# Performance work log

Measured on AMD Instinct MI355X. Metric: run time of the kernel, lower is better.

## Reference

```python
import jax, jax.numpy as jnp
import numpy as np

M = 8192          # flattened tokens (batch*seq)
IN_FEATURES = 4096
OUT_FEATURES = 4096


def setup_inputs() -> dict:
    key = jax.random.key(0)
    k1, k2, k3 = jax.random.split(key, 3)
    # int8-valued activations and weights, stored as int32 (values in [-128, 127])
    x = jax.random.randint(k1, (M, IN_FEATURES), -128, 128, dtype=jnp.int32)
    int_weight = jax.random.randint(k2, (OUT_FEATURES, IN_FEATURES), -128, 127, dtype=jnp.int32)
    bias = (jax.random.normal(k3, (OUT_FEATURES,), dtype=jnp.float32) * 0.02).astype(jnp.float16)
    return {"x": x, "int_weight": int_weight, "bias": bias}


def reference(x, int_weight, bias):
    # x.to(torch.int8); quik int8Matmul: int8 GEMM with int32 accumulation, out = x @ W^T
    x_i8 = x.astype(jnp.int8)
    w_i8 = int_weight.astype(jnp.int8)
    acc = jax.lax.dot_general(
        x_i8, w_i8,
        dimension_numbers=(((1,), (1,)), ((), ())),  # [M, K] x [N, K] -> [M, N]
        preferred_element_type=jnp.int32,
    )
    # .to(torch.float16) then bias add (fused epilogue target)
    return acc.astype(jnp.float16) + bias
```

## Files before the change

kernel.cpp:

```cpp
#include <hip/hip_runtime.h>

#define MDIM 8192
#define NDIM 4096
#define KDIM 4096
#define BM 256
#define BN 256
#define BK 128

typedef int v4i __attribute__((ext_vector_type(4)));
typedef int v16i __attribute__((ext_vector_type(16)));

__device__ __forceinline__ unsigned pack4(int x, int y, int z, int w) {
    return (unsigned)(x & 0xff) | ((unsigned)(y & 0xff) << 8) |
           ((unsigned)(z & 0xff) << 16) | ((unsigned)w << 24);
}

__global__ __launch_bounds__(256) void pack_tiled(const int* __restrict__ x,
                                                  const int* __restrict__ w,
                                                  uint4* __restrict__ xp,
                                                  uint4* __restrict__ wp) {
    __shared__ unsigned lds32[256 * 33];
    const int wg  = blockIdx.x;
    const int tid = threadIdx.x;
    const int kq   = tid & 31;
    const int rsub = tid >> 5;

    const int* src;
    uint4* dst;
    if (wg < 1024) {
        const int mtile = wg >> 5, kiter = wg & 31;
        src = x + (size_t)(mtile * 256) * KDIM + kiter * 128;
        dst = xp + (size_t)(mtile * 32 + kiter) * 2048;
    } else {
        const int ntile = (wg - 1024) >> 5, kiter = wg & 31;
        src = w + (size_t)(ntile * 256) * KDIM + kiter * 128;
        dst = wp + (size_t)(ntile * 32 + kiter) * 2048;
    }
#pragma unroll
    for (int it = 0; it < 32; ++it) {
        const int row = it * 8 + rsub;
        int4 v = *(const int4*)(src + (size_t)row * KDIM + kq * 4);
        lds32[row * 33 + kq] = pack4(v.x, v.y, v.z, v.w);
    }
    __syncthreads();
#pragma unroll
    for (int it = 0; it < 8; ++it) {
        const int g = it * 256 + tid;
        const int kb = g >> 8, row = g & 255;
        const unsigned* p = &lds32[row * 33 + kb * 4];
        uint4 o;
        o.x = p[0]; o.y = p[1]; o.z = p[2]; o.w = p[3];
        dst[g] = o;
    }
}

__global__ __launch_bounds__(512, 2) void gemm_i8_olp(const char* __restrict__ Ap,
                                                      const char* __restrict__ Bp,
                                                      const _Float16* __restrict__ bias,
                                                      _Float16* __restrict__ out) {
    __shared__ __align__(16) char lds[131072];

    const int tid  = threadIdx.x;
    const int lane = tid & 63;
    const int wave = tid >> 6;
    const int wr   = wave >> 2;
    const int wcn  = wave & 3;
    const int l31  = lane & 31;
    const int kg   = lane >> 5;

    const int lid = blockIdx.y * 16 + blockIdx.x;
    const int xc  = lid & 7, ii = lid >> 3;
    const int bx  = (xc & 3) * 4 + (ii & 3);
    const int by  = (xc >> 2) * 16 + (ii >> 2);
    const int bm0 = by * BM;
    const int bn0 = bx * BN;

    const char* apan = Ap + (size_t)by * (BM * KDIM) + tid * 16;
    const char* bpan = Bp + (size_t)bx * (BN * KDIM) + tid * 16;

    int aoff[4], boff[2];
#pragma unroll
    for (int mt = 0; mt < 4; ++mt)
        aoff[mt] = (wr * 128 + mt * 32 + l31) * 16 + kg * 4096;
#pragma unroll
    for (int nt = 0; nt < 2; ++nt)
        boff[nt] = (wcn * 64 + nt * 32 + l31) * 16 + kg * 4096;

    v16i acc[4][2];
#pragma unroll
    for (int mt = 0; mt < 4; ++mt)
#pragma unroll
        for (int nt = 0; nt < 2; ++nt)
#pragma unroll
            for (int i = 0; i < 16; ++i) acc[mt][nt][i] = 0;

    auto stageA = [&](int nb, const char* p) {
#pragma unroll
        for (int c2 = 0; c2 < 4; ++c2)
            __builtin_amdgcn_global_load_lds(
                (__attribute__((address_space(1))) const void*)(p + c2 * 8192),
                (__attribute__((address_space(3))) void*)(lds + nb + c2 * 8192 + tid * 16),
                16, 0, 0);
    };
    auto stageB = [&](int nb, const char* p) {
#pragma unroll
        for (int c2 = 0; c2 < 4; ++c2)
            __builtin_amdgcn_global_load_lds(
                (__attribute__((address_space(1))) const void*)(p + c2 * 8192),
                (__attribute__((address_space(3))) void*)(lds + nb + 32768 + c2 * 8192 + tid * 16),
                16, 0, 0);
    };

    auto mfma8 = [&](const v4i (&af)[4], const v4i (&bfk)[2]) {
        __builtin_amdgcn_s_setprio(1);
#pragma unroll
        for (int mt = 0; mt < 4; ++mt)
#pragma unroll
            for (int nt = 0; nt < 2; ++nt)
                acc[mt][nt] = __builtin_amdgcn_mfma_i32_32x32x32_i8(
                    af[mt], bfk[nt], acc[mt][nt], 0, 0, 0);
        __builtin_amdgcn_s_setprio(0);
    };

    auto tile = [&](int base, int nb, bool stg) {
        asm volatile("s_waitcnt vmcnt(0)" ::: "memory");
        __builtin_amdgcn_s_barrier();
        __builtin_amdgcn_sched_barrier(0);
        if (stg) {
            stageA(nb, apan);
            stageB(nb, bpan);
            apan += BM * BK;
            bpan += BN * BK;
        }
        v4i bf[2][4];
#pragma unroll
        for (int nt = 0; nt < 2; ++nt)
#pragma unroll
            for (int ks = 0; ks < 4; ++ks)
                bf[nt][ks] = *(const v4i*)(lds + base + 32768 + ks * 8192 + boff[nt]);
        v4i afA[4], afB[4];
#pragma unroll
        for (int mt = 0; mt < 4; ++mt)
            afA[mt] = *(const v4i*)(lds + base + aoff[mt]);
        __builtin_amdgcn_sched_barrier(0);
#pragma unroll
        for (int mt = 0; mt < 4; ++mt)
            afB[mt] = *(const v4i*)(lds + base + 8192 + aoff[mt]);
        __builtin_amdgcn_sched_barrier(0);
        {
            v4i bfk[2] = {bf[0][0], bf[1][0]};
            mfma8(afA, bfk);
        }
#pragma unroll
        for (int mt = 0; mt < 4; ++mt)
            afA[mt] = *(const v4i*)(lds + base + 16384 + aoff[mt]);
        __builtin_amdgcn_sched_barrier(0);
        {
            v4i bfk[2] = {bf[0][1], bf[1][1]};
            mfma8(afB, bfk);
        }
#pragma unroll
        for (int mt = 0; mt < 4; ++mt)
            afB[mt] = *(const v4i*)(lds + base + 24576 + aoff[mt]);
        __builtin_amdgcn_sched_barrier(0);
        {
            v4i bfk[2] = {bf[0][2], bf[1][2]};
            mfma8(afA, bfk);
        }
        {
            v4i bfk[2] = {bf[0][3], bf[1][3]};
            mfma8(afB, bfk);
        }
    };

    stageA(0, apan);
    stageB(0, bpan);
    apan += BM * BK;
    bpan += BN * BK;

#pragma unroll 1
    for (int t = 0; t < 31; ++t) {
        const int base = (t & 1) ? 65536 : 0;
        tile(base, base ^ 65536, true);
    }
    tile(65536, 0, false);

    const _Float16 bv0 = bias[bn0 + wcn * 64 + l31];
    const _Float16 bv1 = bias[bn0 + wcn * 64 + 32 + l31];
#pragma unroll
    for (int mt = 0; mt < 4; ++mt) {
#pragma unroll
        for (int nt = 0; nt < 2; ++nt) {
            const int gcol = bn0 + wcn * 64 + nt * 32 + l31;
            const _Float16 bb = nt ? bv1 : bv0;
#pragma unroll
            for (int r = 0; r < 16; ++r) {
                const int rit  = (r & 3) + 8 * (r >> 2) + 4 * kg;
                const int grow = bm0 + wr * 128 + mt * 32 + rit;
                _Float16 h = (_Float16)(float)acc[mt][nt][r] + bb;
                out[(size_t)grow * NDIM + gcol] = h;
            }
        }
    }
}

__global__ __launch_bounds__(256, 2) void gemm_i8_fb(const int* __restrict__ A32,
                                                     const int* __restrict__ B32,
                                                     const _Float16* __restrict__ bias,
                                                     _Float16* __restrict__ out) {
    __shared__ char lds[32768];
    const int tid  = threadIdx.x;
    const int lane = tid & 63;
    const int wave = tid >> 6;
    const int bm0 = blockIdx.y * 256;
    const int bn0 = blockIdx.x * 128;
    const int wr  = wave >> 1;
    const int wc  = wave & 1;
    const int l31 = lane & 31;
    const int kg  = lane >> 5;

    int abase[4];
#pragma unroll
    for (int mt = 0; mt < 4; ++mt)
        abase[mt] = kg * 4096 + (wr * 128 + mt * 32 + l31) * 16;

    v16i acc[4][2];
#pragma unroll
    for (int mt = 0; mt < 4; ++mt)
#pragma unroll
        for (int nt = 0; nt < 2; ++nt)
#pragma unroll
            for (int i = 0; i < 16; ++i) acc[mt][nt][i] = 0;

    int aoffs[8];
#pragma unroll
    for (int r = 0; r < 8; ++r) {
        const int c = r * 4 + wave;
        aoffs[r] = (bm0 + (c & 3) * 64 + lane) * KDIM + (c >> 2) * 16;
    }
    for (int k0 = 0; k0 < KDIM; k0 += 128) {
        v4i bfx[2][4];
#pragma unroll
        for (int r = 0; r < 8; ++r) {
            const int c = r * 4 + wave;
            const int4* s = (const int4*)(A32 + (size_t)aoffs[r]);
            int4 v0 = s[0], v1 = s[1], v2 = s[2], v3 = s[3];
            uint4 pk;
            pk.x = pack4(v0.x, v0.y, v0.z, v0.w);
            pk.y = pack4(v1.x, v1.y, v1.z, v1.w);
            pk.z = pack4(v2.x, v2.y, v2.z, v2.w);
            pk.w = pack4(v3.x, v3.y, v3.z, v3.w);
            *(uint4*)(lds + c * 1024 + lane * 16) = pk;
            aoffs[r] += 128;
        }
#pragma unroll
        for (int nt = 0; nt < 2; ++nt)
#pragma unroll
            for (int ks = 0; ks < 4; ++ks) {
                const int* s = B32 + (size_t)(bn0 + wc * 64 + nt * 32 + l31) * KDIM
                               + k0 + (2 * ks + kg) * 16;
                int4 v0 = ((const int4*)s)[0], v1 = ((const int4*)s)[1];
                int4 v2 = ((const int4*)s)[2], v3 = ((const int4*)s)[3];
                bfx[nt][ks][0] = (int)pack4(v0.x, v0.y, v0.z, v0.w);
                bfx[nt][ks][1] = (int)pack4(v1.x, v1.y, v1.z, v1.w);
                bfx[nt][ks][2] = (int)pack4(v2.x, v2.y, v2.z, v2.w);
                bfx[nt][ks][3] = (int)pack4(v3.x, v3.y, v3.z, v3.w);
            }
        __syncthreads();
#pragma unroll
        for (int ks = 0; ks < 4; ++ks) {
            v4i afr[4];
#pragma unroll
            for (int mt = 0; mt < 4; ++mt)
                afr[mt] = *(const v4i*)(lds + abase[mt] + ks * 8192);
#pragma unroll
            for (int mt = 0; mt < 4; ++mt)
#pragma unroll
                for (int nt = 0; nt < 2; ++nt)
                    acc[mt][nt] = __builtin_amdgcn_mfma_i32_32x32x32_i8(
                        afr[mt], bfx[nt][ks], acc[mt][nt], 0, 0, 0);
        }
        __syncthreads();
    }

    const _Float16 bv0 = bias[bn0 + wc * 64 + l31];
    const _Float16 bv1 = bias[bn0 + wc * 64 + 32 + l31];
#pragma unroll
    for (int mt = 0; mt < 4; ++mt) {
#pragma unroll
        for (int nt = 0; nt < 2; ++nt) {
            const int gcol = bn0 + wc * 64 + nt * 32 + l31;
            const _Float16 bb = nt ? bv1 : bv0;
#pragma unroll
            for (int r = 0; r < 16; ++r) {
                const int rit  = (r & 3) + 8 * (r >> 2) + 4 * kg;
                const int grow = bm0 + wr * 128 + mt * 32 + rit;
                _Float16 h = (_Float16)(float)acc[mt][nt][r] + bb;
                out[(size_t)grow * NDIM + gcol] = h;
            }
        }
    }
}

extern "C" void kernel_launch(void* const* d_in, const int* in_sizes, int n_in,
                              void* d_out, int out_size, void* d_ws, size_t ws_size,
                              hipStream_t stream) {
    const int* x = (const int*)d_in[0];
    const int* w = (const int*)d_in[1];
    const _Float16* bias = (const _Float16*)d_in[2];
    _Float16* out = (_Float16*)d_out;

    const size_t xbytes = (size_t)MDIM * KDIM;
    const size_t wbytes = (size_t)NDIM * KDIM;

    if (ws_size >= xbytes + wbytes) {
        char* xp = (char*)d_ws;
        char* wp = xp + xbytes;
        pack_tiled<<<1536, 256, 0, stream>>>(x, w, (uint4*)xp, (uint4*)wp);
        gemm_i8_olp<<<dim3(NDIM / BN, MDIM / BM), 512, 0, stream>>>(
            (const char*)xp, (const char*)wp, bias, out);
    } else {
        gemm_i8_fb<<<dim3(NDIM / 128, MDIM / 256), 256, 0, stream>>>(
            x, w, bias, out);
    }
}
```

Baseline: 381.5 us.

## Load B fragments directly from global into registers, halve LDS buffers

The GEMM main loop no longer stages the B (weight) tile through LDS. Each wave now loads its B fragments straight from global memory into registers, split into early and late halves, while only A is double-buffered in LDS. LDS use drops from 128 KB to 64 KB, and A reads and MFMAs are software-pipelined across tile boundaries. The aim is to cut LDS traffic and footprint. In exchange, B global loads are duplicated across the waves of a block, and their latency is now exposed inside the compute schedule.

```diff
diff --git a/kernel.cpp b/kernel.cpp
--- a/kernel.cpp
+++ b/kernel.cpp
@@ -54,11 +54,11 @@
     }
 }
 
-__global__ __launch_bounds__(512, 2) void gemm_i8_olp(const char* __restrict__ Ap,
-                                                      const char* __restrict__ Bp,
-                                                      const _Float16* __restrict__ bias,
-                                                      _Float16* __restrict__ out) {
-    __shared__ __align__(16) char lds[131072];
+__global__ __launch_bounds__(512, 2) void gemm_i8_pipe(const char* __restrict__ Ap,
+                                                       const char* __restrict__ Bp,
+                                                       const _Float16* __restrict__ bias,
+                                                       _Float16* __restrict__ out) {
+    __shared__ __align__(16) char lds[65536];
 
     const int tid  = threadIdx.x;
     const int lane = tid & 63;
@@ -76,15 +76,15 @@
     const int bn0 = bx * BN;
 
     const char* apan = Ap + (size_t)by * (BM * KDIM) + tid * 16;
-    const char* bpan = Bp + (size_t)bx * (BN * KDIM) + tid * 16;
-
-    int aoff[4], boff[2];
+    const char* bpan = Bp + (size_t)bx * (BN * KDIM);
+
+    int aoff[4], boffG[2];
 #pragma unroll
     for (int mt = 0; mt < 4; ++mt)
         aoff[mt] = (wr * 128 + mt * 32 + l31) * 16 + kg * 4096;
 #pragma unroll
     for (int nt = 0; nt < 2; ++nt)
-        boff[nt] = (wcn * 64 + nt * 32 + l31) * 16 + kg * 4096;
+        boffG[nt] = (wcn * 64 + nt * 32 + l31) * 16 + kg * 4096;
 
     v16i acc[4][2];
 #pragma unroll
@@ -94,96 +94,96 @@
 #pragma unroll
             for (int i = 0; i < 16; ++i) acc[mt][nt][i] = 0;
 
-    auto stageA = [&](int nb, const char* p) {
+    v4i afP[4], afQ[4];
+    v4i bfE[2][2], bfL[2][2];
+
+    auto stageA = [&](int nb) {
 #pragma unroll
         for (int c2 = 0; c2 < 4; ++c2)
             __builtin_amdgcn_global_load_lds(
-                (__attribute__((address_space(1))) const void*)(p + c2 * 8192),
+                (__attribute__((address_space(1))) const void*)(apan + c2 * 8192),
                 (__attribute__((address_space(3))) void*)(lds + nb + c2 * 8192 + tid * 16),
                 16, 0, 0);
     };
-    auto stageB = [&](int nb, const char* p) {
-#pragma unroll
-        for (int c2 = 0; c2 < 4; ++c2)
-            __builtin_amdgcn_global_load_lds(
-                (__attribute__((address_space(1))) const void*)(p + c2 * 8192),
-                (__attribute__((address_space(3))) void*)(lds + nb + 32768 + c2 * 8192 + tid * 16),
-                16, 0, 0);
+    auto loadB2 = [&](v4i (&d)[2][2], int ksb) {
+#pragma unroll
+        for (int nt = 0; nt < 2; ++nt)
+#pragma unroll
+            for (int k = 0; k < 2; ++k)
+                d[nt][k] = *(const v4i*)(bpan + boffG[nt] + (ksb + k) * 8192);
     };
-
-    auto mfma8 = [&](const v4i (&af)[4], const v4i (&bfk)[2]) {
+    auto readA = [&](v4i (&d)[4], int base, int ks) {
+#pragma unroll
+        for (int mt = 0; mt < 4; ++mt)
+            d[mt] = *(const v4i*)(lds + base + ks * 8192 + aoff[mt]);
+    };
+    auto cl = [&](const v4i (&a)[4], const v4i (&b)[2][2], int k) {
         __builtin_amdgcn_s_setprio(1);
 #pragma unroll
         for (int mt = 0; mt < 4; ++mt)
 #pragma unroll
             for (int nt = 0; nt < 2; ++nt)
                 acc[mt][nt] = __builtin_amdgcn_mfma_i32_32x32x32_i8(
-                    af[mt], bfk[nt], acc[mt][nt], 0, 0, 0);
+                    a[mt], b[nt][k], acc[mt][nt], 0, 0, 0);
         __builtin_amdgcn_s_setprio(0);
     };
 
-    auto tile = [&](int base, int nb, bool stg) {
-        asm volatile("s_waitcnt vmcnt(0)" ::: "memory");
-        __builtin_amdgcn_s_barrier();
-        __builtin_amdgcn_sched_barrier(0);
-        if (stg) {
-            stageA(nb, apan);
-            stageB(nb, bpan);
-            apan += BM * BK;
-            bpan += BN * BK;
-        }
-        v4i bf[2][4];
-#pragma unroll
-        for (int nt = 0; nt < 2; ++nt)
-#pragma unroll
-            for (int ks = 0; ks < 4; ++ks)
-                bf[nt][ks] = *(const v4i*)(lds + base + 32768 + ks * 8192 + boff[nt]);
-        v4i afA[4], afB[4];
-#pragma unroll
-        for (int mt = 0; mt < 4; ++mt)
-            afA[mt] = *(const v4i*)(lds + base + aoff[mt]);
-        __builtin_amdgcn_sched_barrier(0);
-#pragma unroll
-        for (int mt = 0; mt < 4; ++mt)
-            afB[mt] = *(const v4i*)(lds + base + 8192 + aoff[mt]);
-        __builtin_amdgcn_sched_barrier(0);
-        {
-            v4i bfk[2] = {bf[0][0], bf[1][0]};
-            mfma8(afA, bfk);
-        }
-#pragma unroll
-        for (int mt = 0; mt < 4; ++mt)
-            afA[mt] = *(const v4i*)(lds + base + 16384 + aoff[mt]);
-        __builtin_amdgcn_sched_barrier(0);
-        {
-            v4i bfk[2] = {bf[0][1], bf[1][1]};
-            mfma8(afB, bfk);
-        }
-#pragma unroll
-        for (int mt = 0; mt < 4; ++mt)
-            afB[mt] = *(const v4i*)(lds + base + 24576 + aoff[mt]);
-        __builtin_amdgcn_sched_barrier(0);
-        {
-            v4i bfk[2] = {bf[0][2], bf[1][2]};
-            mfma8(afA, bfk);
-        }
-        {
-            v4i bfk[2] = {bf[0][3], bf[1][3]};
-            mfma8(afB, bfk);
-        }
-    };
-
-    stageA(0, apan);
-    stageB(0, bpan);
+#define SB0 __builtin_amdgcn_sched_barrier(0)
+#define TOPBAR do { asm volatile("s_waitcnt vmcnt(0)" ::: "memory"); \
+                    __builtin_amdgcn_s_barrier(); } while (0)
+
+    stageA(0);
+    TOPBAR; SB0;
+    loadB2(bfE, 0);
+    stageA(32768);
     apan += BM * BK;
+    SB0;
+    loadB2(bfL, 2);
+    readA(afP, 0, 0);
+    readA(afQ, 0, 1);
+    SB0;
+    cl(afP, bfE, 0);
+    SB0;
+    readA(afP, 0, 2);
+    SB0;
+    cl(afQ, bfE, 1);
+    SB0;
+    readA(afQ, 0, 3);
     bpan += BN * BK;
+    SB0;
 
 #pragma unroll 1
-    for (int t = 0; t < 31; ++t) {
-        const int base = (t & 1) ? 65536 : 0;
-        tile(base, base ^ 65536, true);
-    }
-    tile(65536, 0, false);
+    for (int t = 1; t < 32; ++t) {
+        const int cur = (t & 1) ? 32768 : 0;
+        TOPBAR; SB0;
+        loadB2(bfE, 0);
+        stageA(cur ^ 32768);
+        apan += BM * BK;
+        SB0;
+        cl(afP, bfL, 0);
+        SB0;
+        readA(afP, cur, 0);
+        SB0;
+        cl(afQ, bfL, 1);
+        SB0;
+        readA(afQ, cur, 1);
+        loadB2(bfL, 2);
+        SB0;
+        cl(afP, bfE, 0);
+        SB0;
+        readA(afP, cur, 2);
+        SB0;
+        cl(afQ, bfE, 1);
+        SB0;
+        readA(afQ, cur, 3);
+        bpan += BN * BK;
+        SB0;
+    }
+    cl(afP, bfL, 0);
+    cl(afQ, bfL, 1);
+
+#undef SB0
+#undef TOPBAR
 
     const _Float16 bv0 = bias[bn0 + wcn * 64 + l31];
     const _Float16 bv1 = bias[bn0 + wcn * 64 + 32 + l31];
@@ -317,7 +317,7 @@
         char* xp = (char*)d_ws;
         char* wp = xp + xbytes;
         pack_tiled<<<1536, 256, 0, stream>>>(x, w, (uint4*)xp, (uint4*)wp);
-        gemm_i8_olp<<<dim3(NDIM / BN, MDIM / BM), 512, 0, stream>>>(
+        gemm_i8_pipe<<<dim3(NDIM / BN, MDIM / BM), 512, 0, stream>>>(
             (const char*)xp, (const char*)wp, bias, out);
     } else {
         gemm_i8_fb<<<dim3(NDIM / 128, MDIM / 256), 256, 0, stream>>>(
```

After: 390.3 us. 2.3% more time.
